# Kernel tuning notes

Measured on AMD Instinct MI355X. Metric: run time of the kernel, lower is better.

Reference implementation:

```python
import jax, jax.numpy as jnp
import numpy as np

N = 50000      # nodes
E = 800000     # edges (avg degree 16)
INDIM = 128
OUTDIM = 64


def setup_inputs() -> dict:
    key = jax.random.key(0)
    k1, k2, k3, k4, k5 = jax.random.split(key, 5)
    h = jax.random.normal(k1, (N, INDIM), dtype=jnp.float32)
    W = jax.random.normal(k2, (INDIM, OUTDIM), dtype=jnp.float32) * 0.05
    Wa = jax.random.normal(k3, (2 * OUTDIM,), dtype=jnp.float32) * 0.05
    src = jax.random.randint(k4, (E,), 0, N)
    dst = jax.random.randint(k5, (E,), 0, N)
    return {"h": h, "W": W, "Wa": Wa, "src": src, "dst": dst}


def reference(h, W, Wa, src, dst):
    # node transform: n_mlp_layer=1, bias=False MultiLinearLayer == one linear
    z = h @ W  # [N, OUTDIM]
    # edge attention: relu(attn_linear(cat(z_src, z_dst)))
    # avoid materializing [E, 2*OUTDIM] concat: split Wa into src/dst halves
    s = z @ Wa[:OUTDIM]   # [N] src contribution
    t = z @ Wa[OUTDIM:]   # [N] dst contribution
    e = jax.nn.relu(s[src] + t[dst])  # [E]
    # segment softmax over incoming edges of each destination node
    m = jax.ops.segment_max(e, dst, num_segments=N)      # [N]
    ex = jnp.exp(e - m[dst])                             # [E]
    denom = jax.ops.segment_sum(ex, dst, num_segments=N) # [N]
    alpha = ex / denom[dst]                              # [E]
    # weighted scatter-sum aggregation of src features (dropout p=0 -> identity)
    h_out = jax.ops.segment_sum(alpha[:, None] * z[src], dst, num_segments=N)
    # batch_norm=False; final activation relu; dropout p=0 -> identity
    return jax.nn.relu(h_out)
```

## Files before the change

kernel.cpp:

```cpp
#include <hip/hip_runtime.h>
#include <math.h>

#define INDIM 128
#define OUTDIM 64
#define HK 136
#define CP 68
#define SCHUNK 2048

typedef __bf16 bf16x8 __attribute__((ext_vector_type(8)));
typedef float f32x4 __attribute__((ext_vector_type(4)));
typedef unsigned short ushortx8 __attribute__((ext_vector_type(8)));

static __device__ __forceinline__ unsigned short f2bf(float f) {
    unsigned u = __float_as_uint(f);
    u += 0x7FFFu + ((u >> 16) & 1u);
    return (unsigned short)(u >> 16);
}
static __device__ __forceinline__ float bf2f(unsigned short b) {
    return __uint_as_float((unsigned)b << 16);
}

__global__ __launch_bounds__(256) void prep(
    const float* __restrict__ W, unsigned short* __restrict__ W2,
    int* __restrict__ bcnt)
{
    int tid = threadIdx.x;
    if (blockIdx.x == 0) {
        bcnt[tid] = 0;
        bcnt[tid + 256] = 0;
        return;
    }
    int e0 = (blockIdx.x - 1) * 512 + tid * 2;
    #pragma unroll
    for (int u = 0; u < 2; ++u) {
        int e = e0 + u;
        int k = e >> 6, n = e & 63;
        unsigned swz = ((unsigned)(n * 256 + 2 * k)) ^ ((unsigned)((n & 7) << 4));
        W2[swz >> 1] = f2bf(W[e]);
    }
}

__global__ __launch_bounds__(256) void nt_count(
    const float* __restrict__ h, const unsigned short* __restrict__ W2,
    const float* __restrict__ Wa, unsigned short* __restrict__ z,
    float* __restrict__ s, float* __restrict__ t,
    const int* __restrict__ dst, int* __restrict__ bcnt,
    int N, int E, int count_blocks)
{
    __shared__ __align__(16) unsigned short smem[64 * HK + 64 * 128];
    unsigned short* As = smem;
    unsigned short* Bs = smem + 64 * HK;
    float* Cs = (float*)smem;
    int tid = threadIdx.x;

    if (blockIdx.x < count_blocks) {
        int* l = (int*)smem;
        l[tid] = 0;
        __syncthreads();
        int base = blockIdx.x * 8192;
        #pragma unroll 2
        for (int u = 0; u < 8; ++u) {
            int i = base + (u * 256 + tid) * 4;
            if (i + 3 < E) {
                int4 d4 = *(const int4*)&dst[i];
                atomicAdd(&l[d4.x >> 8], 1);
                atomicAdd(&l[d4.y >> 8], 1);
                atomicAdd(&l[d4.z >> 8], 1);
                atomicAdd(&l[d4.w >> 8], 1);
            } else {
                for (int q = i; q < E; ++q) atomicAdd(&l[dst[q] >> 8], 1);
            }
        }
        __syncthreads();
        if (l[tid]) atomicAdd(bcnt + tid, l[tid]);
        return;
    }

    int node0 = (blockIdx.x - count_blocks) * 64;
    int nv = min(64, N - node0);
    int wv = tid >> 6, l = tid & 63;

    {
        const float4* hg = (const float4*)(h + (size_t)node0 * INDIM);
        #pragma unroll
        for (int i = 0; i < 8; ++i) {
            int idx = i * 256 + tid;
            int n = idx >> 5, j = idx & 31;
            float4 v = (n < nv) ? hg[n * 32 + j] : make_float4(0.f, 0.f, 0.f, 0.f);
            ushort4 b = make_ushort4(f2bf(v.x), f2bf(v.y), f2bf(v.z), f2bf(v.w));
            *(ushort4*)&As[n * HK + j * 4] = b;
        }
    }
    {
        const unsigned short* gsrc = W2 + wv * 2048;
        unsigned short* lbase = Bs + wv * 2048;
        #pragma unroll
        for (int c = 0; c < 4; ++c) {
            __builtin_amdgcn_global_load_lds(
                (const __attribute__((address_space(1))) unsigned int*)(gsrc + c * 512 + l * 8),
                (__attribute__((address_space(3))) unsigned int*)(lbase + c * 512),
                16, 0, 0);
        }
    }
    __syncthreads();

    int lr = l & 15, lg = l >> 4;

    f32x4 acc[4];
    #pragma unroll
    for (int nf = 0; nf < 4; ++nf) acc[nf] = (f32x4){0.f, 0.f, 0.f, 0.f};

    #pragma unroll
    for (int ks = 0; ks < 4; ++ks) {
        int k0 = ks * 32 + lg * 8;
        bf16x8 a = *(const bf16x8*)&As[(wv * 16 + lr) * HK + k0];
        #pragma unroll
        for (int nf = 0; nf < 4; ++nf) {
            unsigned boff = ((unsigned)((nf * 16 + lr) * 256 + 2 * k0))
                          ^ ((unsigned)((lr & 7) << 4));
            bf16x8 b = *(const bf16x8*)((const char*)Bs + boff);
            acc[nf] = __builtin_amdgcn_mfma_f32_16x16x32_bf16(a, b, acc[nf], 0, 0, 0);
        }
    }

    __syncthreads();

    #pragma unroll
    for (int nf = 0; nf < 4; ++nf)
        #pragma unroll
        for (int r = 0; r < 4; ++r)
            Cs[(wv * 16 + lg * 4 + r) * CP + nf * 16 + lr] = acc[nf][r];

    int row = wv * 16 + (l >> 2);
    int cq = l & 3;
    int node = node0 + row;
    float ssum = 0.f, tsum = 0.f;
    #pragma unroll
    for (int qq = 0; qq < 2; ++qq) {
        int c0 = cq * 16 + qq * 8;
        float4 ca = *(const float4*)&Cs[row * CP + c0];
        float4 cb = *(const float4*)&Cs[row * CP + c0 + 4];
        float4 wsa = *(const float4*)&Wa[c0];
        float4 wsb = *(const float4*)&Wa[c0 + 4];
        float4 wta = *(const float4*)&Wa[OUTDIM + c0];
        float4 wtb = *(const float4*)&Wa[OUTDIM + c0 + 4];
        ssum += ca.x * wsa.x + ca.y * wsa.y + ca.z * wsa.z + ca.w * wsa.w
              + cb.x * wsb.x + cb.y * wsb.y + cb.z * wsb.z + cb.w * wsb.w;
        tsum += ca.x * wta.x + ca.y * wta.y + ca.z * wta.z + ca.w * wta.w
              + cb.x * wtb.x + cb.y * wtb.y + cb.z * wtb.z + cb.w * wtb.w;
        if (node < N) {
            ushortx8 zb;
            zb[0] = f2bf(ca.x); zb[1] = f2bf(ca.y);
            zb[2] = f2bf(ca.z); zb[3] = f2bf(ca.w);
            zb[4] = f2bf(cb.x); zb[5] = f2bf(cb.y);
            zb[6] = f2bf(cb.z); zb[7] = f2bf(cb.w);
            *(ushortx8*)&z[(size_t)node * OUTDIM + c0] = zb;
        }
    }
    ssum += __shfl_xor(ssum, 1, 64);
    ssum += __shfl_xor(ssum, 2, 64);
    tsum += __shfl_xor(tsum, 1, 64);
    tsum += __shfl_xor(tsum, 2, 64);
    if (cq == 0 && node < N) {
        s[node] = ssum;
        t[node] = tsum;
    }
}

__global__ __launch_bounds__(256) void bucket_scatter(
    const int* __restrict__ src, const int* __restrict__ dst,
    const int* __restrict__ bcnt, int* __restrict__ gcursor,
    int* __restrict__ esort, int E)
{
    __shared__ int lcnt[256];
    __shared__ int loff[256];
    __shared__ int gbase[256];
    __shared__ int lcur[256];
    __shared__ int bs[256];
    __shared__ int stage[SCHUNK];
    __shared__ unsigned char bof[SCHUNK];
    int tid = threadIdx.x;
    int base = blockIdx.x * SCHUNK;
    int ne = min(SCHUNK, E - base);

    int bc = bcnt[tid];
    bs[tid] = bc;
    lcnt[tid] = 0;
    __syncthreads();
    for (int off = 1; off < 256; off <<= 1) {
        int add = (tid >= off) ? bs[tid - off] : 0;
        __syncthreads();
        bs[tid] += add;
        __syncthreads();
    }
    int bstart_own = bs[tid] - bc;

    int mys[8], myd[8];
    #pragma unroll
    for (int u = 0; u < 8; ++u) {
        int li = u * 256 + tid;
        if (li < ne) {
            mys[u] = src[base + li];
            myd[u] = dst[base + li];
            atomicAdd(&lcnt[myd[u] >> 8], 1);
        } else myd[u] = -1;
    }
    __syncthreads();

    loff[tid] = lcnt[tid];
    __syncthreads();
    for (int off = 1; off < 256; off <<= 1) {
        int add = (tid >= off) ? loff[tid - off] : 0;
        __syncthreads();
        loff[tid] += add;
        __syncthreads();
    }
    int excl = loff[tid] - lcnt[tid];
    loff[tid] = excl;
    lcur[tid] = excl;
    if (lcnt[tid] > 0)
        gbase[tid] = bstart_own + atomicAdd(gcursor + tid, lcnt[tid]);
    __syncthreads();

    #pragma unroll
    for (int u = 0; u < 8; ++u) {
        if (myd[u] >= 0) {
            int b = myd[u] >> 8;
            int p = atomicAdd(&lcur[b], 1);
            stage[p] = ((myd[u] & 255) << 24) | mys[u];
            bof[p] = (unsigned char)b;
        }
    }
    __syncthreads();

    for (int i = tid; i < ne; i += 256) {
        int b = bof[i];
        esort[gbase[b] + (i - loff[b])] = stage[i];
    }
}

__global__ __launch_bounds__(256) void bucket_fill(
    const int* __restrict__ esort, const int* __restrict__ bcnt,
    int* __restrict__ counts, int* __restrict__ offsets,
    int* __restrict__ srcs, int N)
{
    __shared__ int bs[256];
    __shared__ int cnt[256];
    __shared__ int off[256];
    __shared__ int cur[256];
    int tid = threadIdx.x;
    int b = blockIdx.x;

    int bc = bcnt[tid];
    bs[tid] = bc;
    cnt[tid] = 0;
    __syncthreads();
    for (int o = 1; o < 256; o <<= 1) {
        int add = (tid >= o) ? bs[tid - o] : 0;
        __syncthreads();
        bs[tid] += add;
        __syncthreads();
    }
    int e0 = (b > 0) ? bs[b - 1] : 0;
    int e1 = bs[b];
    int node0 = b << 8;

    for (int i = e0 + tid; i < e1; i += 256)
        atomicAdd(&cnt[((unsigned)esort[i]) >> 24], 1);
    __syncthreads();

    off[tid] = cnt[tid];
    __syncthreads();
    for (int o = 1; o < 256; o <<= 1) {
        int add = (tid >= o) ? off[tid - o] : 0;
        __syncthreads();
        off[tid] += add;
        __syncthreads();
    }
    int excl = off[tid] - cnt[tid];
    cur[tid] = excl;
    int node = node0 + tid;
    if (node < N) { counts[node] = cnt[tid]; offsets[node] = e0 + excl; }
    __syncthreads();

    for (int i = e0 + tid; i < e1; i += 256) {
        int pe = esort[i];
        int p = atomicAdd(&cur[((unsigned)pe) >> 24], 1);
        srcs[e0 + p] = pe & 0xFFFFFF;
    }
}

__global__ __launch_bounds__(256) void aggregate(
    const unsigned short* __restrict__ z, const int* __restrict__ srcs,
    const float* __restrict__ s, const float* __restrict__ t,
    const int* __restrict__ offsets, const int* __restrict__ counts,
    float* __restrict__ out, int N)
{
    __shared__ int   ls[8][64];
    __shared__ float le[8][64];
    int hw = threadIdx.x >> 5;
    int lane = threadIdx.x & 31;
    int node = blockIdx.x * 8 + hw;
    if (node >= N) return;
    int start = offsets[node];
    int deg = counts[node];
    float2 acc = make_float2(0.f, 0.f);

    if (deg > 0) {
        float tn = t[node];
        float se = 0.f;
        for (int c0 = 0; c0 < deg; c0 += 64) {
            int cn = min(64, deg - c0);
            float pe = 0.f;
            if (lane < cn) {
                int sj = srcs[start + c0 + lane];
                float e = __expf(fmaxf(s[sj] + tn, 0.f));
                ls[hw][lane] = sj; le[hw][lane] = e; pe += e;
            }
            if (lane + 32 < cn) {
                int sj = srcs[start + c0 + lane + 32];
                float e = __expf(fmaxf(s[sj] + tn, 0.f));
                ls[hw][lane + 32] = sj; le[hw][lane + 32] = e; pe += e;
            }
            #pragma unroll
            for (int off = 16; off; off >>= 1) pe += __shfl_xor(pe, off, 32);
            se += pe;

            int j = 0;
            for (; j + 8 <= cn; j += 8) {
                int si[8]; float ei[8]; ushort2 ai[8];
                #pragma unroll
                for (int u = 0; u < 8; ++u) { si[u] = ls[hw][j + u]; ei[u] = le[hw][j + u]; }
                #pragma unroll
                for (int u = 0; u < 8; ++u)
                    ai[u] = *(const ushort2*)&z[(size_t)si[u] * OUTDIM + lane * 2];
                #pragma unroll
                for (int u = 0; u < 8; ++u) {
                    acc.x += ei[u] * bf2f(ai[u].x);
                    acc.y += ei[u] * bf2f(ai[u].y);
                }
            }
            for (; j < cn; ++j) {
                int sj = ls[hw][j]; float ej = le[hw][j];
                ushort2 a = *(const ushort2*)&z[(size_t)sj * OUTDIM + lane * 2];
                acc.x += ej * bf2f(a.x);
                acc.y += ej * bf2f(a.y);
            }
        }
        float inv = 1.f / se;
        acc.x = fmaxf(acc.x * inv, 0.f);
        acc.y = fmaxf(acc.y * inv, 0.f);
    }
    *(float2*)&out[(size_t)node * OUTDIM + lane * 2] = acc;
}

extern "C" void kernel_launch(void* const* d_in, const int* in_sizes, int n_in,
                              void* d_out, int out_size, void* d_ws, size_t ws_size,
                              hipStream_t stream) {
    const float* h  = (const float*)d_in[0];
    const float* W  = (const float*)d_in[1];
    const float* Wa = (const float*)d_in[2];
    const int* src  = (const int*)d_in[3];
    const int* dst  = (const int*)d_in[4];
    int N = in_sizes[0] / INDIM;
    int E = in_sizes[3];
    float* out = (float*)d_out;
    int nbuck = (N + 255) >> 8;

    char* ws = (char*)d_ws;
    unsigned short* z = (unsigned short*)ws;  ws += (size_t)N * OUTDIM * 2;
    float* s       = (float*)ws;  ws += (size_t)N * 4;
    float* t       = (float*)ws;  ws += (size_t)N * 4;
    int*   srcs    = (int*)ws;    ws += (size_t)E * 4;
    int*   counts  = (int*)ws;    ws += (size_t)N * 4;
    int*   offsets = (int*)ws;    ws += (size_t)N * 4;
    int*   esort   = (int*)ws;    ws += (size_t)E * 4;
    int*   bcnt    = (int*)ws;    ws += 256 * 4;
    int*   gcursor = (int*)ws;    ws += 256 * 4;
    unsigned short* W2 = (unsigned short*)ws; ws += INDIM * OUTDIM * 2;

    int gemm_blocks = (N + 63) / 64;
    int count_blocks = (E + 8191) / 8192;

    prep<<<17, 256, 0, stream>>>(W, W2, bcnt);

    nt_count<<<gemm_blocks + count_blocks, 256, 0, stream>>>(
        h, W2, Wa, z, s, t, dst, bcnt, N, E, count_blocks);
    bucket_scatter<<<(E + SCHUNK - 1) / SCHUNK, 256, 0, stream>>>(
        src, dst, bcnt, gcursor, esort, E);
    bucket_fill<<<nbuck, 256, 0, stream>>>(esort, bcnt, counts, offsets, srcs, N);
    aggregate<<<(N + 7) / 8, 256, 0, stream>>>(z, srcs, s, t, offsets, counts, out, N);
}
```

Baseline: 136.4 us.

## Vectorize edge loads, cache bucket edges in LDS, pack offset/count pairs

In bucket_scatter, src and dst are now read as int4 vectors instead of scalar ints, with a scalar fallback at the tail. bucket_fill copies each bucket's sorted edges into shared memory (up to FCAP entries), so the second pass reads LDS instead of reading global memory again. A path for oversized buckets keeps the old double global read. Per-node offsets and counts are packed into one int2 array, so aggregate issues a single 8-byte load per node. The risks are the int4 alignment assumption on the chunk base and the extra LDS per block, which may lower occupancy.

```diff
diff --git a/kernel.cpp b/kernel.cpp
--- a/kernel.cpp
+++ b/kernel.cpp
@@ -6,6 +6,7 @@
 #define HK 136
 #define CP 68
 #define SCHUNK 2048
+#define FCAP 5376
 
 typedef __bf16 bf16x8 __attribute__((ext_vector_type(8)));
 typedef float f32x4 __attribute__((ext_vector_type(4)));
@@ -196,14 +197,33 @@
     int bstart_own = bs[tid] - bc;
 
     int mys[8], myd[8];
-    #pragma unroll
-    for (int u = 0; u < 8; ++u) {
-        int li = u * 256 + tid;
-        if (li < ne) {
-            mys[u] = src[base + li];
-            myd[u] = dst[base + li];
-            atomicAdd(&lcnt[myd[u] >> 8], 1);
-        } else myd[u] = -1;
+    const int4* src4 = (const int4*)(src + base);
+    const int4* dst4 = (const int4*)(dst + base);
+    #pragma unroll
+    for (int u = 0; u < 2; ++u) {
+        int li0 = (u * 256 + tid) * 4;
+        if (li0 + 3 < ne) {
+            int4 sv = src4[u * 256 + tid];
+            int4 dv = dst4[u * 256 + tid];
+            mys[u * 4 + 0] = sv.x; myd[u * 4 + 0] = dv.x;
+            mys[u * 4 + 1] = sv.y; myd[u * 4 + 1] = dv.y;
+            mys[u * 4 + 2] = sv.z; myd[u * 4 + 2] = dv.z;
+            mys[u * 4 + 3] = sv.w; myd[u * 4 + 3] = dv.w;
+            atomicAdd(&lcnt[dv.x >> 8], 1);
+            atomicAdd(&lcnt[dv.y >> 8], 1);
+            atomicAdd(&lcnt[dv.z >> 8], 1);
+            atomicAdd(&lcnt[dv.w >> 8], 1);
+        } else {
+            #pragma unroll
+            for (int q = 0; q < 4; ++q) {
+                int li = li0 + q;
+                if (li < ne) {
+                    mys[u * 4 + q] = src[base + li];
+                    myd[u * 4 + q] = dst[base + li];
+                    atomicAdd(&lcnt[myd[u * 4 + q] >> 8], 1);
+                } else myd[u * 4 + q] = -1;
+            }
+        }
     }
     __syncthreads();
 
@@ -241,13 +261,13 @@
 
 __global__ __launch_bounds__(256) void bucket_fill(
     const int* __restrict__ esort, const int* __restrict__ bcnt,
-    int* __restrict__ counts, int* __restrict__ offsets,
-    int* __restrict__ srcs, int N)
+    int2* __restrict__ cofs, int* __restrict__ srcs, int N)
 {
     __shared__ int bs[256];
     __shared__ int cnt[256];
     __shared__ int off[256];
     __shared__ int cur[256];
+    __shared__ int es[FCAP];
     int tid = threadIdx.x;
     int b = blockIdx.x;
 
@@ -263,38 +283,67 @@
     }
     int e0 = (b > 0) ? bs[b - 1] : 0;
     int e1 = bs[b];
+    int ne = e1 - e0;
     int node0 = b << 8;
 
-    for (int i = e0 + tid; i < e1; i += 256)
-        atomicAdd(&cnt[((unsigned)esort[i]) >> 24], 1);
-    __syncthreads();
-
-    off[tid] = cnt[tid];
-    __syncthreads();
-    for (int o = 1; o < 256; o <<= 1) {
-        int add = (tid >= o) ? off[tid - o] : 0;
-        __syncthreads();
-        off[tid] += add;
-        __syncthreads();
-    }
-    int excl = off[tid] - cnt[tid];
-    cur[tid] = excl;
-    int node = node0 + tid;
-    if (node < N) { counts[node] = cnt[tid]; offsets[node] = e0 + excl; }
-    __syncthreads();
-
-    for (int i = e0 + tid; i < e1; i += 256) {
-        int pe = esort[i];
-        int p = atomicAdd(&cur[((unsigned)pe) >> 24], 1);
-        srcs[e0 + p] = pe & 0xFFFFFF;
+    if (ne <= FCAP) {
+        for (int i = tid; i < ne; i += 256) {
+            int pe = esort[e0 + i];
+            es[i] = pe;
+            atomicAdd(&cnt[((unsigned)pe) >> 24], 1);
+        }
+        __syncthreads();
+
+        off[tid] = cnt[tid];
+        __syncthreads();
+        for (int o = 1; o < 256; o <<= 1) {
+            int add = (tid >= o) ? off[tid - o] : 0;
+            __syncthreads();
+            off[tid] += add;
+            __syncthreads();
+        }
+        int excl = off[tid] - cnt[tid];
+        cur[tid] = excl;
+        int node = node0 + tid;
+        if (node < N) cofs[node] = make_int2(e0 + excl, cnt[tid]);
+        __syncthreads();
+
+        for (int i = tid; i < ne; i += 256) {
+            int pe = es[i];
+            int p = atomicAdd(&cur[((unsigned)pe) >> 24], 1);
+            srcs[e0 + p] = pe & 0xFFFFFF;
+        }
+    } else {
+        for (int i = e0 + tid; i < e1; i += 256)
+            atomicAdd(&cnt[((unsigned)esort[i]) >> 24], 1);
+        __syncthreads();
+
+        off[tid] = cnt[tid];
+        __syncthreads();
+        for (int o = 1; o < 256; o <<= 1) {
+            int add = (tid >= o) ? off[tid - o] : 0;
+            __syncthreads();
+            off[tid] += add;
+            __syncthreads();
+        }
+        int excl = off[tid] - cnt[tid];
+        cur[tid] = excl;
+        int node = node0 + tid;
+        if (node < N) cofs[node] = make_int2(e0 + excl, cnt[tid]);
+        __syncthreads();
+
+        for (int i = e0 + tid; i < e1; i += 256) {
+            int pe = esort[i];
+            int p = atomicAdd(&cur[((unsigned)pe) >> 24], 1);
+            srcs[e0 + p] = pe & 0xFFFFFF;
+        }
     }
 }
 
 __global__ __launch_bounds__(256) void aggregate(
     const unsigned short* __restrict__ z, const int* __restrict__ srcs,
     const float* __restrict__ s, const float* __restrict__ t,
-    const int* __restrict__ offsets, const int* __restrict__ counts,
-    float* __restrict__ out, int N)
+    const int2* __restrict__ cofs, float* __restrict__ out, int N)
 {
     __shared__ int   ls[8][64];
     __shared__ float le[8][64];
@@ -302,8 +351,9 @@
     int lane = threadIdx.x & 31;
     int node = blockIdx.x * 8 + hw;
     if (node >= N) return;
-    int start = offsets[node];
-    int deg = counts[node];
+    int2 oc = cofs[node];
+    int start = oc.x;
+    int deg = oc.y;
     float2 acc = make_float2(0.f, 0.f);
 
     if (deg > 0) {
@@ -372,8 +422,7 @@
     float* s       = (float*)ws;  ws += (size_t)N * 4;
     float* t       = (float*)ws;  ws += (size_t)N * 4;
     int*   srcs    = (int*)ws;    ws += (size_t)E * 4;
-    int*   counts  = (int*)ws;    ws += (size_t)N * 4;
-    int*   offsets = (int*)ws;    ws += (size_t)N * 4;
+    int2*  cofs    = (int2*)ws;   ws += (size_t)N * 8;
     int*   esort   = (int*)ws;    ws += (size_t)E * 4;
     int*   bcnt    = (int*)ws;    ws += 256 * 4;
     int*   gcursor = (int*)ws;    ws += 256 * 4;
@@ -388,6 +437,6 @@
         h, W2, Wa, z, s, t, dst, bcnt, N, E, count_blocks);
     bucket_scatter<<<(E + SCHUNK - 1) / SCHUNK, 256, 0, stream>>>(
         src, dst, bcnt, gcursor, esort, E);
-    bucket_fill<<<nbuck, 256, 0, stream>>>(esort, bcnt, counts, offsets, srcs, N);
-    aggregate<<<(N + 7) / 8, 256, 0, stream>>>(z, srcs, s, t, offsets, counts, out, N);
-}
+    bucket_fill<<<nbuck, 256, 0, stream>>>(esort, bcnt, cofs, srcs, N);
+    aggregate<<<(N + 7) / 8, 256, 0, stream>>>(z, srcs, s, t, cofs, out, N);
+}
```

New measurement: 132.6 us, median of 2. 2.8% less time.
